# Kernel tuning notes

Hardware: AMD Instinct MI355X
Metric: run time of the kernel (lower is better)

## Reference

```python
import jax, jax.numpy as jnp
import numpy as np
import math

S, D = 8192, 128

def setup_inputs() -> dict:
    key = jax.random.key(0)
    kq, kk, kv = jax.random.split(key, 3)
    return {
        "q": jax.random.normal(kq, (S, D), dtype=jnp.float32),
        "k": jax.random.normal(kk, (S, D), dtype=jnp.float32),
        "v": jax.random.normal(kv, (S, D), dtype=jnp.float32),
    }

def reference(q, k, v):
    # scores: [S, S]; scale by sqrt(d) as in the torch module
    scale = 1.0 / math.sqrt(q.shape[1])
    scores = (q @ k.T) * scale
    attn = jax.nn.softmax(scores, axis=-1)
    return attn @ v
```

## Files before the change

### kernel.cpp

```cpp
#include <hip/hip_runtime.h>
#include <hip/hip_bf16.h>

#define SEQ 8192
#define HD 128
#define BM 128
#define BN 64
#define NQT (SEQ / BM)
#define THREADS 512

typedef __bf16 bf16_t;
typedef __bf16 bf16x2 __attribute__((ext_vector_type(2)));
typedef __bf16 bf16x8 __attribute__((ext_vector_type(8)));
typedef float f32x4 __attribute__((ext_vector_type(4)));
typedef float f32x16 __attribute__((ext_vector_type(16)));
typedef unsigned int u32x4 __attribute__((ext_vector_type(4)));

#if __has_builtin(__builtin_amdgcn_exp2f)
__device__ inline float exp2_fast(float x) { return __builtin_amdgcn_exp2f(x); }
#else
__device__ inline float exp2_fast(float x) { return exp2f(x); }
#endif

__device__ inline void load_lds16(const void* g, void* l) {
  __builtin_amdgcn_global_load_lds(
      (const __attribute__((address_space(1))) void*)g,
      (__attribute__((address_space(3))) void*)l, 16, 0, 0);
}

__global__ __launch_bounds__(256) void prep_kernel(const float* __restrict__ K,
                                                   const float* __restrict__ V,
                                                   bf16_t* __restrict__ Kb,
                                                   bf16_t* __restrict__ VT) {
  const int b = (int)blockIdx.x;
  const int tid = (int)threadIdx.x;
  if (b < 256) {
    __shared__ float tile[64][65];
    const int T = b & 127;
    const int d0 = (b >> 7) * 64;
    const int s0 = T * 64;
    const int r = tid >> 2;
    const int c0 = (tid & 3) * 16;
#pragma unroll
    for (int j4 = 0; j4 < 4; ++j4) {
      float4 x = *(const float4*)&V[(size_t)(s0 + r) * HD + d0 + c0 + j4 * 4];
      tile[r][c0 + j4 * 4 + 0] = x.x;
      tile[r][c0 + j4 * 4 + 1] = x.y;
      tile[r][c0 + j4 * 4 + 2] = x.z;
      tile[r][c0 + j4 * 4 + 3] = x.w;
    }
    __syncthreads();
    const int d_l = tid & 63;
    const int kc0 = (tid >> 6) * 2;
#pragma unroll
    for (int k2 = 0; k2 < 2; ++k2) {
      const int kc = kc0 + k2;
      bf16x8 wv;
#pragma unroll
      for (int j = 0; j < 8; ++j) wv[j] = (bf16_t)tile[kc * 8 + j][d_l];
      *(bf16x8*)&VT[((size_t)(T * 8 + kc) * 128 + d0 + d_l) * 8] = wv;
    }
  } else {
    const int base = (b - 256) * 2048 + tid * 8;
    const int row = base >> 7;
    const int c = (base >> 3) & 15;
    const int T = row >> 6;
    const int r = row & 63;
    float4 a = *(const float4*)&K[base];
    float4 cc = *(const float4*)&K[base + 4];
    bf16x8 f;
    f[0] = (bf16_t)a.x; f[1] = (bf16_t)a.y; f[2] = (bf16_t)a.z; f[3] = (bf16_t)a.w;
    f[4] = (bf16_t)cc.x; f[5] = (bf16_t)cc.y; f[6] = (bf16_t)cc.z; f[7] = (bf16_t)cc.w;
    *(bf16x8*)&Kb[((size_t)(T * 16 + c) * 64 + r) * 8] = f;
  }
}

__global__ __launch_bounds__(THREADS, 4) void fattn_kernel(
    const float* __restrict__ Q, const bf16_t* __restrict__ Kb,
    const bf16_t* __restrict__ VT, float* __restrict__ OpartT,
    float* __restrict__ Lpart, int kshift, int nit) {
  __shared__ __align__(16) bf16_t kt2[2][16][64][8];
  __shared__ __align__(16) bf16_t vt2[2][8][128][8];
  __shared__ __align__(16) char pbuf[4][4][64][16];

  const int tid = (int)threadIdx.x;
  const int lane = tid & 63;
  const int w = tid >> 6;
  const int qw = w & 3;
  const int g = w >> 2;
  const int h = lane >> 5;
  const int n32 = lane & 31;

  const int qt = (int)blockIdx.x >> kshift;
  const int sp = (int)blockIdx.x & ((1 << kshift) - 1);
  const int qbase = qt * BM;
  const int tile0 = sp * nit;

  const float SC2 = 0.08838834764831845f * 1.4426950408889634f;

  bf16x8 qf[8];
  {
    const float* qp = Q + (size_t)(qbase + qw * 32 + n32) * HD + h * 8;
#pragma unroll
    for (int kk = 0; kk < 8; ++kk) {
      float4 a = *(const float4*)(qp + kk * 16);
      float4 b = *(const float4*)(qp + kk * 16 + 4);
      bf16x8 f;
      f[0] = (bf16_t)(a.x * SC2); f[1] = (bf16_t)(a.y * SC2);
      f[2] = (bf16_t)(a.z * SC2); f[3] = (bf16_t)(a.w * SC2);
      f[4] = (bf16_t)(b.x * SC2); f[5] = (bf16_t)(b.y * SC2);
      f[6] = (bf16_t)(b.z * SC2); f[7] = (bf16_t)(b.w * SC2);
      qf[kk] = f;
    }
  }

  f32x16 o_acc[2];
#pragma unroll
  for (int i = 0; i < 2; ++i)
#pragma unroll
    for (int e = 0; e < 16; ++e) o_acc[i][e] = 0.f;
  float l_acc = 0.f;

  const bf16_t* ksrc[2];
  const bf16_t* vsrc[2];
  char* kdst[2];
  char* vdst[2];
#pragma unroll
  for (int t = 0; t < 2; ++t) {
    const int rr = w * 2 + t;
    ksrc[t] = Kb + ((size_t)(tile0 * 16 + rr) * 64 + lane) * 8;
    vsrc[t] = VT + ((size_t)(tile0 * 8 + (rr >> 1)) * 128 + (rr & 1) * 64 + lane) * 8;
    kdst[t] = (char*)&kt2[0][0][0][0] + rr * 1024;
    vdst[t] = (char*)&vt2[0][0][0][0] + rr * 1024;
  }

#pragma unroll
  for (int t = 0; t < 2; ++t) {
    load_lds16(ksrc[t], kdst[t]);
    load_lds16(vsrc[t], vdst[t]);
    ksrc[t] += 8192;
    vsrc[t] += 8192;
  }
  __syncthreads();

  const bf16_t* ktb = &kt2[0][h][g * 32 + n32][0];
  const bf16_t* vtbA = &vt2[0][h][g * 64 + n32][0];
  int bo = 0;
  int nb = 16384;

  for (int it = 0; it < nit; ++it) {
    if (it + 1 < nit) {
#pragma unroll
      for (int t = 0; t < 2; ++t) {
        load_lds16(ksrc[t], kdst[t] + nb);
        load_lds16(vsrc[t], vdst[t] + nb);
        ksrc[t] += 8192;
        vsrc[t] += 8192;
      }
    }

    const bf16_t* kc_ = ktb + bo;
    f32x16 sacc;
#pragma unroll
    for (int e = 0; e < 16; ++e) sacc[e] = 0.f;
#pragma unroll
    for (int kk = 0; kk < 8; ++kk) {
      bf16x8 af = *(const bf16x8*)(kc_ + kk * 1024);
      sacc = __builtin_amdgcn_mfma_f32_32x32x16_bf16(af, qf[kk], sacc, 0, 0, 0);
    }

    bf16x8 pown[2];
#pragma unroll
    for (int kk2 = 0; kk2 < 2; ++kk2) {
      float pf[8];
#pragma unroll
      for (int j = 0; j < 8; ++j) pf[j] = exp2_fast(sacc[8 * kk2 + j]);
#pragma unroll
      for (int j = 0; j < 8; ++j) l_acc += pf[j];
      bf16x2 p0, p1, p2, p3;
      p0[0] = (bf16_t)pf[0]; p0[1] = (bf16_t)pf[1];
      p1[0] = (bf16_t)pf[2]; p1[1] = (bf16_t)pf[3];
      p2[0] = (bf16_t)pf[4]; p2[1] = (bf16_t)pf[5];
      p3[0] = (bf16_t)pf[6]; p3[1] = (bf16_t)pf[7];
      const unsigned int sA = __builtin_bit_cast(unsigned int, p0);
      const unsigned int sB = __builtin_bit_cast(unsigned int, p1);
      const unsigned int sC = __builtin_bit_cast(unsigned int, p2);
      const unsigned int sD = __builtin_bit_cast(unsigned int, p3);
      unsigned int s0 = h ? sA : sC, s1 = h ? sB : sD;
      unsigned int r0 = __shfl_xor(s0, 32);
      unsigned int r1 = __shfl_xor(s1, 32);
      unsigned int o0 = h ? sC : sA, o1 = h ? sD : sB;
      u32x4 fv;
      fv[0] = h ? r0 : o0; fv[1] = h ? r1 : o1;
      fv[2] = h ? o0 : r0; fv[3] = h ? o1 : r1;
      pown[kk2] = __builtin_bit_cast(bf16x8, fv);
      *(u32x4*)&pbuf[qw][g * 2 + kk2][lane][0] = fv;
    }

    asm volatile("s_waitcnt lgkmcnt(0)\n\ts_barrier" ::: "memory");

    const bf16_t* vc_ = vtbA + bo;
#pragma unroll
    for (int c = 0; c < 4; ++c) {
      bf16x8 pb = ((c >> 1) == g) ? pown[c & 1]
                                  : *(const bf16x8*)&pbuf[qw][c][lane][0];
#pragma unroll
      for (int dt = 0; dt < 2; ++dt) {
        bf16x8 av = *(const bf16x8*)(vc_ + (2 * c) * 1024 + dt * 256);
        o_acc[dt] = __builtin_amdgcn_mfma_f32_32x32x16_bf16(av, pb, o_acc[dt], 0, 0, 0);
      }
    }

    __syncthreads();
    bo ^= 8192;
    nb ^= 16384;
  }

  {
    float* op = OpartT + (size_t)sp * HD * SEQ + qbase + qw * 32 + n32;
#pragma unroll
    for (int dt = 0; dt < 2; ++dt)
#pragma unroll
      for (int reg = 0; reg < 16; ++reg) {
        const int d = g * 64 + dt * 32 + (reg & 3) + 8 * (reg >> 2) + 4 * h;
        op[(size_t)d * SEQ] = o_acc[dt][reg];
      }
    float l = l_acc + __shfl_xor(l_acc, 32);
    float* lfb = (float*)pbuf;
    if (lane < 32) lfb[g * 128 + qw * 32 + n32] = l;
    __syncthreads();
    if (g == 0 && lane < 32)
      Lpart[(size_t)sp * SEQ + qbase + qw * 32 + n32] = l + lfb[128 + qw * 32 + n32];
  }
}

__global__ __launch_bounds__(256) void combine_kernel(const float* __restrict__ OpartT,
                                                      const float* __restrict__ Lpart,
                                                      float* __restrict__ out, int ksplit) {
  __shared__ float tile[64][68];
  __shared__ float lbuf[64];
  const int tid = (int)threadIdx.x;
  const int q0 = (int)blockIdx.x * 64;
  if (tid < 64) {
    float s = 0.f;
    for (int sp = 0; sp < ksplit; ++sp) s += Lpart[(size_t)sp * SEQ + q0 + tid];
    lbuf[tid] = 1.0f / s;
  }
  __syncthreads();
  const int dd = tid >> 2, qc = tid & 3;
  const int q = tid >> 2, dc = tid & 3;
  for (int db = 0; db < 2; ++db) {
    f32x4 acc[4];
#pragma unroll
    for (int jj = 0; jj < 4; ++jj)
#pragma unroll
      for (int e = 0; e < 4; ++e) acc[jj][e] = 0.f;
    for (int sp = 0; sp < ksplit; ++sp) {
      const float* src = OpartT + ((size_t)sp * HD + db * 64 + dd) * SEQ + q0 + qc * 16;
#pragma unroll
      for (int jj = 0; jj < 4; ++jj) {
        f32x4 v = *(const f32x4*)(src + jj * 4);
#pragma unroll
        for (int e = 0; e < 4; ++e) acc[jj][e] += v[e];
      }
    }
#pragma unroll
    for (int jj = 0; jj < 4; ++jj) *(f32x4*)&tile[dd][qc * 16 + jj * 4] = acc[jj];
    __syncthreads();
    const float inv = lbuf[q];
#pragma unroll
    for (int jj = 0; jj < 4; ++jj) {
      f32x4 r;
#pragma unroll
      for (int i = 0; i < 4; ++i) r[i] = tile[dc * 16 + jj * 4 + i][q] * inv;
      *(f32x4*)&out[(size_t)(q0 + q) * HD + db * 64 + dc * 16 + jj * 4] = r;
    }
    __syncthreads();
  }
}

extern "C" void kernel_launch(void* const* d_in, const int* in_sizes, int n_in,
                              void* d_out, int out_size, void* d_ws, size_t ws_size,
                              hipStream_t stream) {
  const float* Q = (const float*)d_in[0];
  const float* K = (const float*)d_in[1];
  const float* V = (const float*)d_in[2];
  float* out = (float*)d_out;

  int ksplit = 8, kshift = 3;
  while (ksplit > 1) {
    size_t need = (size_t)ksplit * SEQ * HD * 4
                + (size_t)ksplit * SEQ * 4
                + (size_t)SEQ * HD * 2 * 2;
    if (need <= ws_size) break;
    ksplit >>= 1; kshift--;
  }

  char* ws = (char*)d_ws;
  float* OpartT = (float*)ws;
  float* Lpart = (float*)(ws + (size_t)ksplit * SEQ * HD * 4);
  bf16_t* Kb = (bf16_t*)(ws + (size_t)ksplit * SEQ * HD * 4 + (size_t)ksplit * SEQ * 4);
  bf16_t* VT = Kb + (size_t)SEQ * HD;

  const int nit = SEQ / (ksplit * BN);

  prep_kernel<<<768, 256, 0, stream>>>(K, V, Kb, VT);
  fattn_kernel<<<NQT * ksplit, THREADS, 0, stream>>>(Q, Kb, VT, OpartT, Lpart, kshift, nit);
  combine_kernel<<<SEQ / 64, 256, 0, stream>>>(OpartT, Lpart, out, ksplit);
}
```

Baseline: 123.1 us.

## Double Q tile to 256 rows and software-pipeline PV one iteration behind QK

Raises the block to 1024 threads covering 256 query rows, so each loaded K/V tile is reused by twice as many queries. The loop is skewed so the P·V MFMAs for the previous tile run in the same iteration as the QK/exp for the current tile. V gets a triple buffer and P a double buffer, which removes one barrier per iteration. This uses much more LDS and allows fewer resident blocks, and with 32 query tiles instead of 64 the grid shape and split balance change.

```diff
diff --git a/kernel.cpp b/kernel.cpp
--- a/kernel.cpp
+++ b/kernel.cpp
@@ -3,10 +3,10 @@
 
 #define SEQ 8192
 #define HD 128
-#define BM 128
+#define BM 256
 #define BN 64
 #define NQT (SEQ / BM)
-#define THREADS 512
+#define THREADS 1024
 
 typedef __bf16 bf16_t;
 typedef __bf16 bf16x2 __attribute__((ext_vector_type(2)));
@@ -78,15 +78,15 @@
     const float* __restrict__ Q, const bf16_t* __restrict__ Kb,
     const bf16_t* __restrict__ VT, float* __restrict__ OpartT,
     float* __restrict__ Lpart, int kshift, int nit) {
-  __shared__ __align__(16) bf16_t kt2[2][16][64][8];
-  __shared__ __align__(16) bf16_t vt2[2][8][128][8];
-  __shared__ __align__(16) char pbuf[4][4][64][16];
+  __shared__ __align__(16) bf16_t kt[2 * 8192];
+  __shared__ __align__(16) bf16_t vt[3 * 8192];
+  __shared__ __align__(16) char pbc[2 * 32768];
 
   const int tid = (int)threadIdx.x;
   const int lane = tid & 63;
   const int w = tid >> 6;
-  const int qw = w & 3;
-  const int g = w >> 2;
+  const int qw = w & 7;
+  const int g = w >> 3;
   const int h = lane >> 5;
   const int n32 = lane & 31;
 
@@ -120,99 +120,92 @@
     for (int e = 0; e < 16; ++e) o_acc[i][e] = 0.f;
   float l_acc = 0.f;
 
-  const bf16_t* ksrc[2];
-  const bf16_t* vsrc[2];
-  char* kdst[2];
-  char* vdst[2];
-#pragma unroll
-  for (int t = 0; t < 2; ++t) {
-    const int rr = w * 2 + t;
-    ksrc[t] = Kb + ((size_t)(tile0 * 16 + rr) * 64 + lane) * 8;
-    vsrc[t] = VT + ((size_t)(tile0 * 8 + (rr >> 1)) * 128 + (rr & 1) * 64 + lane) * 8;
-    kdst[t] = (char*)&kt2[0][0][0][0] + rr * 1024;
-    vdst[t] = (char*)&vt2[0][0][0][0] + rr * 1024;
-  }
-
-#pragma unroll
-  for (int t = 0; t < 2; ++t) {
-    load_lds16(ksrc[t], kdst[t]);
-    load_lds16(vsrc[t], vdst[t]);
-    ksrc[t] += 8192;
-    vsrc[t] += 8192;
-  }
+  const bf16_t* ksrc = Kb + ((size_t)(tile0 * 16 + w) * 64 + lane) * 8;
+  const bf16_t* vsrc = VT + ((size_t)(tile0 * 8 + (w >> 1)) * 128 + (w & 1) * 64 + lane) * 8;
+  char* kdstb = (char*)kt + w * 1024;
+  char* vdstb = (char*)vt + w * 1024;
+
+  load_lds16(ksrc, kdstb);
+  load_lds16(vsrc, vdstb);
+  ksrc += 8192;
+  vsrc += 8192;
   __syncthreads();
 
-  const bf16_t* ktb = &kt2[0][h][g * 32 + n32][0];
-  const bf16_t* vtbA = &vt2[0][h][g * 64 + n32][0];
-  int bo = 0;
-  int nb = 16384;
-
-  for (int it = 0; it < nit; ++it) {
+  const bf16_t* ktb = kt + (g * 32 + n32) * 8 + h * 512;
+  const bf16_t* vtb = vt + (g * 64 + n32) * 8 + h * 1024;
+  char* pbw = pbc + w * 2048 + lane * 16;
+  const char* pbr = pbc + qw * 2048 + lane * 16;
+
+  int kt_ro = 0;
+  int ktd = 16384;
+  int v_pv = 16384, v_nx = 0, v_fr = 8192;
+  int p_wo = 0;
+
+  for (int it = 0; it <= nit; ++it) {
     if (it + 1 < nit) {
-#pragma unroll
-      for (int t = 0; t < 2; ++t) {
-        load_lds16(ksrc[t], kdst[t] + nb);
-        load_lds16(vsrc[t], vdst[t] + nb);
-        ksrc[t] += 8192;
-        vsrc[t] += 8192;
-      }
-    }
-
-    const bf16_t* kc_ = ktb + bo;
-    f32x16 sacc;
-#pragma unroll
-    for (int e = 0; e < 16; ++e) sacc[e] = 0.f;
-#pragma unroll
-    for (int kk = 0; kk < 8; ++kk) {
-      bf16x8 af = *(const bf16x8*)(kc_ + kk * 1024);
-      sacc = __builtin_amdgcn_mfma_f32_32x32x16_bf16(af, qf[kk], sacc, 0, 0, 0);
-    }
-
-    bf16x8 pown[2];
-#pragma unroll
-    for (int kk2 = 0; kk2 < 2; ++kk2) {
-      float pf[8];
-#pragma unroll
-      for (int j = 0; j < 8; ++j) pf[j] = exp2_fast(sacc[8 * kk2 + j]);
-#pragma unroll
-      for (int j = 0; j < 8; ++j) l_acc += pf[j];
-      bf16x2 p0, p1, p2, p3;
-      p0[0] = (bf16_t)pf[0]; p0[1] = (bf16_t)pf[1];
-      p1[0] = (bf16_t)pf[2]; p1[1] = (bf16_t)pf[3];
-      p2[0] = (bf16_t)pf[4]; p2[1] = (bf16_t)pf[5];
-      p3[0] = (bf16_t)pf[6]; p3[1] = (bf16_t)pf[7];
-      const unsigned int sA = __builtin_bit_cast(unsigned int, p0);
-      const unsigned int sB = __builtin_bit_cast(unsigned int, p1);
-      const unsigned int sC = __builtin_bit_cast(unsigned int, p2);
-      const unsigned int sD = __builtin_bit_cast(unsigned int, p3);
-      unsigned int s0 = h ? sA : sC, s1 = h ? sB : sD;
-      unsigned int r0 = __shfl_xor(s0, 32);
-      unsigned int r1 = __shfl_xor(s1, 32);
-      unsigned int o0 = h ? sC : sA, o1 = h ? sD : sB;
-      u32x4 fv;
-      fv[0] = h ? r0 : o0; fv[1] = h ? r1 : o1;
-      fv[2] = h ? o0 : r0; fv[3] = h ? o1 : r1;
-      pown[kk2] = __builtin_bit_cast(bf16x8, fv);
-      *(u32x4*)&pbuf[qw][g * 2 + kk2][lane][0] = fv;
-    }
-
-    asm volatile("s_waitcnt lgkmcnt(0)\n\ts_barrier" ::: "memory");
-
-    const bf16_t* vc_ = vtbA + bo;
-#pragma unroll
-    for (int c = 0; c < 4; ++c) {
-      bf16x8 pb = ((c >> 1) == g) ? pown[c & 1]
-                                  : *(const bf16x8*)&pbuf[qw][c][lane][0];
-#pragma unroll
-      for (int dt = 0; dt < 2; ++dt) {
-        bf16x8 av = *(const bf16x8*)(vc_ + (2 * c) * 1024 + dt * 256);
-        o_acc[dt] = __builtin_amdgcn_mfma_f32_32x32x16_bf16(av, pb, o_acc[dt], 0, 0, 0);
-      }
-    }
-
-    __syncthreads();
-    bo ^= 8192;
-    nb ^= 16384;
+      load_lds16(ksrc, kdstb + ktd);
+      load_lds16(vsrc, vdstb + 2 * v_fr);
+      ksrc += 8192;
+      vsrc += 8192;
+    }
+
+    if (it < nit) {
+      const bf16_t* kr = ktb + kt_ro;
+      f32x16 sacc;
+#pragma unroll
+      for (int e = 0; e < 16; ++e) sacc[e] = 0.f;
+#pragma unroll
+      for (int kk = 0; kk < 8; ++kk) {
+        bf16x8 af = *(const bf16x8*)(kr + kk * 1024);
+        sacc = __builtin_amdgcn_mfma_f32_32x32x16_bf16(af, qf[kk], sacc, 0, 0, 0);
+      }
+#pragma unroll
+      for (int kk2 = 0; kk2 < 2; ++kk2) {
+        float pf[8];
+#pragma unroll
+        for (int j = 0; j < 8; ++j) pf[j] = exp2_fast(sacc[8 * kk2 + j]);
+#pragma unroll
+        for (int j = 0; j < 8; ++j) l_acc += pf[j];
+        bf16x2 p0, p1, p2, p3;
+        p0[0] = (bf16_t)pf[0]; p0[1] = (bf16_t)pf[1];
+        p1[0] = (bf16_t)pf[2]; p1[1] = (bf16_t)pf[3];
+        p2[0] = (bf16_t)pf[4]; p2[1] = (bf16_t)pf[5];
+        p3[0] = (bf16_t)pf[6]; p3[1] = (bf16_t)pf[7];
+        const unsigned int sA = __builtin_bit_cast(unsigned int, p0);
+        const unsigned int sB = __builtin_bit_cast(unsigned int, p1);
+        const unsigned int sC = __builtin_bit_cast(unsigned int, p2);
+        const unsigned int sD = __builtin_bit_cast(unsigned int, p3);
+        unsigned int s0 = h ? sA : sC, s1 = h ? sB : sD;
+        unsigned int r0 = __shfl_xor(s0, 32);
+        unsigned int r1 = __shfl_xor(s1, 32);
+        unsigned int o0 = h ? sC : sA, o1 = h ? sD : sB;
+        u32x4 fv;
+        fv[0] = h ? r0 : o0; fv[1] = h ? r1 : o1;
+        fv[2] = h ? o0 : r0; fv[3] = h ? o1 : r1;
+        *(u32x4*)(pbw + p_wo + kk2 * 1024) = fv;
+      }
+    }
+
+    if (it > 0) {
+      const bf16_t* vr = vtb + v_pv;
+      const char* pr = pbr + (p_wo ^ 32768);
+#pragma unroll
+      for (int c = 0; c < 4; ++c) {
+        bf16x8 pb = *(const bf16x8*)(pr + (c >> 1) * 16384 + (c & 1) * 1024);
+#pragma unroll
+        for (int dt = 0; dt < 2; ++dt) {
+          bf16x8 av = *(const bf16x8*)(vr + c * 2048 + dt * 256);
+          o_acc[dt] = __builtin_amdgcn_mfma_f32_32x32x16_bf16(av, pb, o_acc[dt], 0, 0, 0);
+        }
+      }
+    }
+
+    if (it < nit) __syncthreads();
+
+    kt_ro ^= 8192;
+    ktd ^= 16384;
+    int tswp = v_pv; v_pv = v_nx; v_nx = v_fr; v_fr = tswp;
+    p_wo ^= 32768;
   }
 
   {
@@ -225,11 +218,13 @@
         op[(size_t)d * SEQ] = o_acc[dt][reg];
       }
     float l = l_acc + __shfl_xor(l_acc, 32);
-    float* lfb = (float*)pbuf;
-    if (lane < 32) lfb[g * 128 + qw * 32 + n32] = l;
+    __syncthreads();
+    float* lfb = (float*)pbc;
+    if (lane < 32) lfb[g * 256 + qw * 32 + n32] = l;
     __syncthreads();
     if (g == 0 && lane < 32)
-      Lpart[(size_t)sp * SEQ + qbase + qw * 32 + n32] = l + lfb[128 + qw * 32 + n32];
+      Lpart[(size_t)sp * SEQ + qbase + qw * 32 + n32] =
+          l + lfb[256 + qw * 32 + n32];
   }
 }
 
```

New measurement: 122.4 us. No clear change (-0.5%).
